# Performance work log

Hardware: AMD Instinct MI355X
Metric: run time of the kernel (lower is better)

## Reference

```python
import jax, jax.numpy as jnp
import numpy as np
import math

DEPTH = 3
RATIO = 0.5
EPS = 1e-5


def _mlp_ln(h, W1, b1, W2, b2, W3, b3, g, beta):
    h = jax.nn.gelu(h @ W1 + b1, approximate=False)
    h = jax.nn.gelu(h @ W2 + b2, approximate=False)
    h = h @ W3 + b3
    mu = jnp.mean(h, axis=-1, keepdims=True)
    var = jnp.mean((h - mu) ** 2, axis=-1, keepdims=True)
    return g * (h - mu) * jax.lax.rsqrt(var + EPS) + beta


def _node_to_node(x, s, r, n, p):
    # two-way gather -> scatter_add -> MLP+LN. Row n of x_pad is a zero dummy
    # node that absorbs edges dropped by pooling (fixed-size, jit-friendly).
    x_pad = jnp.concatenate([x, jnp.zeros((1, x.shape[1]), x.dtype)], axis=0)
    msg = x_pad[jnp.concatenate([s, r])]            # [2E, C]
    recv = jnp.concatenate([r, s])                  # [2E]
    agg = jax.ops.segment_sum(msg, recv, num_segments=n + 1)[:n]
    return _mlp_ln(agg, *p)


def _forward(x, senders, receivers, pool_w, down_p, up_p):
    s, r = senders, receivers
    xs, edges, perms = [x], [(s, r)], []
    n = x.shape[0]
    for i in range(DEPTH):
        k = math.ceil(RATIO * n)  # PyG topk: ceil(ratio * N)
        w = pool_w[i]
        score = jnp.tanh(x @ w / jnp.linalg.norm(w))
        vals, perm = jax.lax.top_k(score, k)
        x = x[perm] * vals[:, None]
        # remap edges; dropped nodes (and old dummy n) map to new dummy k
        nmap = jnp.full((n + 1,), k, dtype=s.dtype).at[perm].set(
            jnp.arange(k, dtype=s.dtype))
        ns_, nr_ = nmap[s], nmap[r]
        invalid = (ns_ == k) | (nr_ == k)
        s = jnp.where(invalid, k, ns_)
        r = jnp.where(invalid, k, nr_)
        x = _node_to_node(x, s, r, k, down_p[i])
        if i < DEPTH - 1:
            xs.append(x)
            edges.append((s, r))
        perms.append(perm)
        n = k
    for i in range(DEPTH):
        j = DEPTH - 1 - i
        res = xs[j]
        s, r = edges[j]
        perm = perms[j]
        up = jnp.zeros_like(res).at[perm].set(x)
        x = jnp.concatenate([res, up], axis=-1)  # sum_res=False -> concat
        x = _node_to_node(x, s, r, res.shape[0], up_p[i])
    return x


def setup_inputs() -> dict:
    key = jax.random.key(0)
    ks = jax.random.split(key, 16)
    N, E, C, D = 50000, 600000, 128, DEPTH
    f32 = jnp.float32

    def lin(k, fi, fo):
        return (jax.random.normal(k, (D, fi, fo), f32) / np.sqrt(fi)).astype(f32)

    return {
        'x': jax.random.normal(ks[0], (N, C), f32),
        'senders': jax.random.randint(ks[1], (E,), 0, N, dtype=jnp.int32),
        'receivers': jax.random.randint(ks[2], (E,), 0, N, dtype=jnp.int32),
        'pool_w': jax.random.normal(ks[3], (D, C), f32),
        'down_W1': lin(ks[4], C, C), 'down_b1': jnp.zeros((D, C), f32),
        'down_W2': lin(ks[5], C, C), 'down_b2': jnp.zeros((D, C), f32),
        'down_W3': lin(ks[6], C, C), 'down_b3': jnp.zeros((D, C), f32),
        'down_g': jnp.ones((D, C), f32), 'down_beta': jnp.zeros((D, C), f32),
        'up_W1': lin(ks[7], 2 * C, C), 'up_b1': jnp.zeros((D, C), f32),
        'up_W2': lin(ks[8], C, C), 'up_b2': jnp.zeros((D, C), f32),
        'up_W3': lin(ks[9], C, C), 'up_b3': jnp.zeros((D, C), f32),
        'up_g': jnp.ones((D, C), f32), 'up_beta': jnp.zeros((D, C), f32),
    }


def reference(x, senders, receivers, pool_w,
              down_W1, down_b1, down_W2, down_b2, down_W3, down_b3,
              down_g, down_beta,
              up_W1, up_b1, up_W2, up_b2, up_W3, up_b3, up_g, up_beta):
    down_p = [(down_W1[i], down_b1[i], down_W2[i], down_b2[i],
               down_W3[i], down_b3[i], down_g[i], down_beta[i])
              for i in range(DEPTH)]
    up_p = [(up_W1[i], up_b1[i], up_W2[i], up_b2[i],
             up_W3[i], up_b3[i], up_g[i], up_beta[i])
            for i in range(DEPTH)]
    return _forward(x, senders, receivers, pool_w, down_p, up_p)
```

## Files before the change

### kernel.cpp

```cpp
#include <hip/hip_runtime.h>
#include <math.h>


typedef unsigned short u16;
typedef short bf16x8 __attribute__((ext_vector_type(8)));
typedef float f32x4 __attribute__((ext_vector_type(4)));

#define HIST_STRIDE (2 * 65536 + 512)

__device__ __forceinline__ unsigned int fkey(float f) {
  unsigned int b = __float_as_uint(f);
  return (b & 0x80000000u) ? ~b : (b | 0x80000000u);
}

__device__ __forceinline__ float gelu_f(float v) {
  return 0.5f * v * (1.0f + erff(v * 0.70710678118654752f));
}

__device__ __forceinline__ u16 f2bf(float f) {
  unsigned u = __float_as_uint(f);
  u = (u + 0x7FFFu + ((u >> 16) & 1u)) >> 16;
  return (u16)u;
}
__device__ __forceinline__ float bf2f(u16 u) {
  return __uint_as_float(((unsigned)u) << 16);
}

__global__ void score_kernel(const float* __restrict__ x, const float* __restrict__ w,
                             float* __restrict__ key, float* __restrict__ valt, int n) {
  int wave = threadIdx.x >> 6, lane = threadIdx.x & 63;
  int i = blockIdx.x * 4 + wave;
  if (i >= n) return;
  float2 xv = *(const float2*)&x[(size_t)i * 128 + lane * 2];
  float2 wv = *(const float2*)&w[lane * 2];
  double d  = (double)xv.x * wv.x + (double)xv.y * wv.y;
  double nw = (double)wv.x * wv.x + (double)wv.y * wv.y;
  for (int o = 32; o; o >>= 1) { d += __shfl_down(d, o, 64); nw += __shfl_down(nw, o, 64); }
  if (lane == 0) {
    key[i]  = (float)d;
    valt[i] = (float)tanh(d / sqrt(nw));
  }
}

__global__ void preamble_kernel(const float* __restrict__ x, u16* __restrict__ xb, int n,
                                const float* __restrict__ uW1, const float* __restrict__ uW2,
                                const float* __restrict__ uW3, u16* __restrict__ wt1,
                                u16* __restrict__ wt2, u16* __restrict__ wt3,
                                const float* __restrict__ poolw, double* __restrict__ sqn,
                                u16* __restrict__ z0, u16* __restrict__ z1,
                                u16* __restrict__ z2, int* __restrict__ histAll,
                                int* __restrict__ degAll, int nbX, int nbHZ, int nHist,
                                int nDeg) {
  int b = blockIdx.x;
  if (b < nbX) {
    int gid = b * 256 + threadIdx.x;
    if (gid < n * 32) {
      float4 a = *(const float4*)&x[(size_t)gid * 4];
      *(ushort4*)&xb[(size_t)gid * 4] =
          make_ushort4(f2bf(a.x), f2bf(a.y), f2bf(a.z), f2bf(a.w));
    }
    return;
  }
  b -= nbX;
  if (b < 768) {
    int i = b * 256 + threadIdx.x;
    int lvl = i >> 16, rem = i & 65535;
    if (rem < 32768) {
      int k = rem >> 7, c = rem & 127;
      wt1[(size_t)lvl * 32768 + c * 256 + k] = f2bf(uW1[(size_t)lvl * 32768 + rem]);
    } else if (rem < 49152) {
      int j = rem - 32768; int k = j >> 7, c = j & 127;
      wt2[(size_t)lvl * 16384 + c * 128 + k] = f2bf(uW2[(size_t)lvl * 16384 + j]);
    } else {
      int j = rem - 49152; int k = j >> 7, c = j & 127;
      wt3[(size_t)lvl * 16384 + c * 128 + k] = f2bf(uW3[(size_t)lvl * 16384 + j]);
    }
    return;
  }
  b -= 768;
  if (b == 0) {
    if (threadIdx.x < 64) {
      int lane = threadIdx.x;
      for (int l = 0; l < 3; ++l) {
        float2 wv = *(const float2*)&poolw[l * 128 + lane * 2];
        double nw = (double)wv.x * wv.x + (double)wv.y * wv.y;
        for (int o = 32; o; o >>= 1) nw += __shfl_down(nw, o, 64);
        if (lane == 0) sqn[l] = sqrt(nw);
      }
    }
    return;
  }
  b -= 1;
  if (b == 0) {
    int t = threadIdx.x;
    if (t < 128) { z0[t] = 0; z1[t] = 0; z2[t] = 0; }
    return;
  }
  b -= 1;
  if (b < nbHZ) {
    int i = b * 256 + threadIdx.x;
    if (i < nHist) histAll[i] = 0;
    return;
  }
  b -= nbHZ;
  {
    int i = b * 256 + threadIdx.x;
    if (i < nDeg) degAll[i] = 0;
  }
}

__global__ void hist_hi_kernel(const float* __restrict__ key, int* __restrict__ hist,
                               int* __restrict__ csum, int n) {
  __shared__ int lc[256];
  lc[threadIdx.x] = 0;
  __syncthreads();
  int i = blockIdx.x * 256 + threadIdx.x;
  if (i < n) {
    unsigned b = fkey(key[i]) >> 16;
    atomicAdd(&hist[b], 1);
    atomicAdd(&lc[b >> 8], 1);
  }
  __syncthreads();
  int v = lc[threadIdx.x];
  if (v) atomicAdd(&csum[threadIdx.x], v);
}

__global__ void hist_lo_kernel(const float* __restrict__ key, const int* __restrict__ meta,
                               int* __restrict__ hist, int* __restrict__ csum, int n) {
  __shared__ int lc[256];
  lc[threadIdx.x] = 0;
  __syncthreads();
  int i = blockIdx.x * 256 + threadIdx.x;
  if (i < n) {
    unsigned u = fkey(key[i]);
    if ((u >> 16) == (unsigned)meta[0]) {
      unsigned b = u & 0xFFFFu;
      atomicAdd(&hist[b], 1);
      atomicAdd(&lc[b >> 8], 1);
    }
  }
  __syncthreads();
  int v = lc[threadIdx.x];
  if (v) atomicAdd(&csum[threadIdx.x], v);
}

__global__ void find_hi2_kernel(const int* __restrict__ hist, const int* __restrict__ csum,
                                int* __restrict__ meta, int k) {
  __shared__ int s[256];
  __shared__ int cSh, cumSh;
  int t = threadIdx.x;
  s[t] = csum[t];
  __syncthreads();
  if (t == 0) {
    int cum = 0, c = 0;
    for (int i = 255; i >= 0; --i) {
      if (cum + s[i] >= k) { c = i; break; }
      cum += s[i];
    }
    cSh = c; cumSh = cum;
  }
  __syncthreads();
  int c = cSh;
  s[t] = hist[c * 256 + t];
  __syncthreads();
  if (t == 0) {
    int cum = cumSh;
    for (int b = 255; b >= 0; --b) {
      int v = s[b];
      if (cum + v >= k) { meta[0] = c * 256 + b; meta[1] = k - cum; break; }
      cum += v;
    }
  }
}

__global__ void find_lo2_kernel(const int* __restrict__ hist, const int* __restrict__ csum,
                                int* __restrict__ meta) {
  __shared__ int s[256];
  __shared__ int cSh, cumSh;
  int t = threadIdx.x;
  int m = meta[1], B = meta[0];
  s[t] = csum[t];
  __syncthreads();
  if (t == 0) {
    int cum = 0, c = 0;
    for (int i = 255; i >= 0; --i) {
      if (cum + s[i] >= m) { c = i; break; }
      cum += s[i];
    }
    cSh = c; cumSh = cum;
  }
  __syncthreads();
  int c = cSh;
  s[t] = hist[c * 256 + t];
  __syncthreads();
  if (t == 0) {
    int cum = cumSh;
    for (int b = 255; b >= 0; --b) {
      int v = s[b];
      if (cum + v >= m) {
        meta[3] = (int)((((unsigned)B) << 16) | (unsigned)(c * 256 + b));
        meta[4] = m - cum;
        break;
      }
      cum += v;
    }
    meta[5] = 0;
  }
}

__global__ void tie_count_kernel(const float* __restrict__ key, const int* __restrict__ meta,
                                 int* __restrict__ tcnt, int n) {
  __shared__ int cnt[4];
  unsigned uT = (unsigned)meta[3];
  int i = blockIdx.x * 256 + threadIdx.x;
  bool tie = (i < n) && (fkey(key[i]) == uT);
  unsigned long long m = __ballot(tie);
  int lane = threadIdx.x & 63, w = threadIdx.x >> 6;
  if (lane == 0) cnt[w] = __popcll(m);
  __syncthreads();
  if (threadIdx.x == 0) tcnt[blockIdx.x] = cnt[0] + cnt[1] + cnt[2] + cnt[3];
}

__global__ void tie_select_kernel(const float* __restrict__ key, const float* __restrict__ valt,
                                  const int* __restrict__ tcnt, int* __restrict__ meta,
                                  int* __restrict__ perm, float* __restrict__ vals,
                                  int* __restrict__ nmap, int n, int k) {
  __shared__ int red[256];
  __shared__ int woff[4];
  int t = threadIdx.x;
  red[t] = (t < (int)blockIdx.x) ? tcnt[t] : 0;
  __syncthreads();
  for (int s = 128; s; s >>= 1) {
    if (t < s) red[t] += red[t + s];
    __syncthreads();
  }
  int blockbase = red[0];
  unsigned uT = (unsigned)meta[3];
  int tsel = meta[4];
  int i = blockIdx.x * 256 + t;
  unsigned u = (i < n) ? fkey(key[i]) : 0u;
  bool tie = (i < n) && (u == uT);
  unsigned long long m = __ballot(tie);
  int lane = t & 63, w = t >> 6;
  if (lane == 0) woff[w] = __popcll(m);
  __syncthreads();
  if (t == 0) {
    int c = 0;
    for (int q = 0; q < 4; ++q) { int v = woff[q]; woff[q] = c; c += v; }
  }
  __syncthreads();
  if (i > n) return;
  if (i == n) { nmap[n] = k; return; }
  bool sel;
  if (tie) {
    int pre = __popcll(m & ((1ull << lane) - 1ull));
    int rank = blockbase + woff[w] + pre;
    sel = (rank < tsel);
  } else {
    sel = (u > uT);
  }
  if (sel) {
    int slot = atomicAdd(&meta[5], 1);
    perm[slot] = i; vals[slot] = valt[i]; nmap[i] = slot;
  } else {
    nmap[i] = k;
  }
}

__global__ void pool_kernel(const float* __restrict__ x, const int* __restrict__ perm,
                            const float* __restrict__ vals, float* __restrict__ xp, int k) {
  int gid = blockIdx.x * 256 + threadIdx.x;
  int t = gid >> 5;
  if (t >= k) return;
  int c = (gid & 31) << 2;
  float v = vals[t];
  float4 a = *(const float4*)&x[(size_t)perm[t] * 128 + c];
  a.x *= v; a.y *= v; a.z *= v; a.w *= v;
  *(float4*)&xp[(size_t)t * 128 + c] = a;
}

__global__ void remap_deg_rank_kernel(const int* __restrict__ s_in, const int* __restrict__ r_in,
                                      const int* __restrict__ nmap, int* __restrict__ s_out,
                                      int* __restrict__ r_out, int* __restrict__ deg,
                                      int* __restrict__ rkS, int* __restrict__ rkR,
                                      int E, int k) {
  int e = blockIdx.x * 256 + threadIdx.x;
  if (e >= E) return;
  int a = nmap[s_in[e]], b = nmap[r_in[e]];
  if (a == k || b == k) { a = k; b = k; }
  s_out[e] = a; r_out[e] = b;
  if (a < k) {
    rkR[e] = atomicAdd(&deg[b], 1);
    rkS[e] = atomicAdd(&deg[a], 1);
  }
}

__global__ void deg_rank_kernel(const int* __restrict__ s, const int* __restrict__ r,
                                int* __restrict__ deg, int* __restrict__ rkS,
                                int* __restrict__ rkR, int E, int n) {
  int e = blockIdx.x * 256 + threadIdx.x;
  if (e >= E) return;
  int ss = s[e];
  if (ss >= n) return;
  int rr = r[e];
  rkR[e] = atomicAdd(&deg[rr], 1);
  rkS[e] = atomicAdd(&deg[ss], 1);
}

__global__ void scan_part_kernel(const int* __restrict__ deg, int* __restrict__ bsum, int n) {
  __shared__ int l[256];
  int i = blockIdx.x * 256 + threadIdx.x;
  l[threadIdx.x] = (i < n) ? deg[i] : 0;
  __syncthreads();
  for (int s = 128; s; s >>= 1) {
    if (threadIdx.x < s) l[threadIdx.x] += l[threadIdx.x + s];
    __syncthreads();
  }
  if (threadIdx.x == 0) bsum[blockIdx.x] = l[0];
}

__global__ void scan_final_kernel(const int* __restrict__ deg, const int* __restrict__ bsum,
                                  int* __restrict__ off, int n) {
  __shared__ int red[256];
  __shared__ int l[256];
  int i = blockIdx.x * 256 + threadIdx.x;
  int t = threadIdx.x;
  red[t] = (t < (int)blockIdx.x) ? bsum[t] : 0;
  __syncthreads();
  for (int s = 128; s; s >>= 1) {
    if (t < s) red[t] += red[t + s];
    __syncthreads();
  }
  int base = red[0];
  int v = (i < n) ? deg[i] : 0;
  l[t] = v;
  __syncthreads();
#pragma unroll
  for (int s = 1; s < 256; s <<= 1) {
    int add = (t >= s) ? l[t - s] : 0;
    __syncthreads();
    l[t] += add;
    __syncthreads();
  }
  int incl = l[t];
  if (i < n) {
    int e = base + incl - v;
    off[i] = e;
    if (i == n - 1) off[n] = base + incl;
  }
}

__global__ void rank_scatter_kernel(const int* __restrict__ s, const int* __restrict__ r,
                                    const int* __restrict__ off, const int* __restrict__ rkS,
                                    const int* __restrict__ rkR, int* __restrict__ idx,
                                    int E, int n) {
  int e = blockIdx.x * 256 + threadIdx.x;
  if (e >= E) return;
  int ss = s[e];
  if (ss >= n) return;
  int rr = r[e];
  idx[off[rr] + rkR[e]] = ss;
  idx[off[ss] + rkS[e]] = rr;
}

__global__ void idxup3_kernel(const int* __restrict__ idxA, const int* __restrict__ nmA,
                              const int* __restrict__ lenA, int* __restrict__ outA,
                              const int* __restrict__ idxB, const int* __restrict__ nmB,
                              const int* __restrict__ lenB, int* __restrict__ outB,
                              const int* __restrict__ idxC, const int* __restrict__ nmC,
                              const int* __restrict__ lenC, int* __restrict__ outC,
                              int nbSeg, int maxlen) {
  int seg = blockIdx.x / nbSeg;
  int j = (blockIdx.x - seg * nbSeg) * 256 + threadIdx.x;
  if (j >= maxlen) return;
  const int* idx; const int* nm; const int* len; int* out;
  if (seg == 0)      { idx = idxA; nm = nmA; len = lenA; out = outA; }
  else if (seg == 1) { idx = idxB; nm = nmB; len = lenB; out = outB; }
  else               { idx = idxC; nm = nmC; len = lenC; out = outC; }
  if (j >= len[0]) return;
  out[j] = nm[idx[j]];
}

__global__ void agg_kernel(const float* __restrict__ x, const int* __restrict__ off,
                           const int* __restrict__ idx, float* __restrict__ agg, int n) {
  int wave = threadIdx.x >> 6, lane = threadIdx.x & 63;
  int v = blockIdx.x * 4 + wave;
  if (v >= n) return;
  int lo = __builtin_amdgcn_readfirstlane(off[v]);
  int hi = __builtin_amdgcn_readfirstlane(off[v + 1]);
  int g = lane >> 5, sl = lane & 31;
  const float* bp = x + sl * 4;
  float4 acc = {0.f, 0.f, 0.f, 0.f};
#define ACC_F(EE)                                        \
  do {                                                   \
    float4 w_ = *(const float4*)(bp + (size_t)(EE) * 128);\
    acc.x += w_.x; acc.y += w_.y; acc.z += w_.z; acc.w += w_.w; \
  } while (0)
  int j = lo;
  for (; j + 8 <= hi; j += 8) {
    int q0 = idx[j],     q1 = idx[j + 1], q2 = idx[j + 2], q3 = idx[j + 3];
    int q4 = idx[j + 4], q5 = idx[j + 5], q6 = idx[j + 6], q7 = idx[j + 7];
    ACC_F(g ? q1 : q0);
    ACC_F(g ? q3 : q2);
    ACC_F(g ? q5 : q4);
    ACC_F(g ? q7 : q6);
  }
  for (; j + 2 <= hi; j += 2) {
    int q0 = idx[j], q1 = idx[j + 1];
    ACC_F(g ? q1 : q0);
  }
  if (j < hi) {
    int q0 = idx[j];
    if (!g) ACC_F(q0);
  }
#undef ACC_F
  acc.x += __shfl_xor(acc.x, 32, 64);
  acc.y += __shfl_xor(acc.y, 32, 64);
  acc.z += __shfl_xor(acc.z, 32, 64);
  acc.w += __shfl_xor(acc.w, 32, 64);
  if (!g) *(float4*)&agg[(size_t)v * 128 + sl * 4] = acc;
}

template <int OFS>
__global__ void agg_gather_kernel(const u16* __restrict__ tab, const int* __restrict__ idx,
                                  const int* __restrict__ off, u16* __restrict__ agg, int n) {
  int wave = threadIdx.x >> 6, lane = threadIdx.x & 63;
  int v = blockIdx.x * 4 + wave;
  if (v >= n) return;
  int lo = __builtin_amdgcn_readfirstlane(off[v]);
  int hi = __builtin_amdgcn_readfirstlane(off[v + 1]);
  int g = lane >> 4, sl = lane & 15;
  const u16* bp = tab + sl * 8;
  float4 a0 = {0.f, 0.f, 0.f, 0.f}, a1 = {0.f, 0.f, 0.f, 0.f};

#define ACC_ROW(EE)                                     \
  do {                                                  \
    uint4 wq = *(const uint4*)(bp + (size_t)(EE) * 128);\
    a0.x += __uint_as_float(wq.x << 16);                \
    a0.y += __uint_as_float(wq.x & 0xffff0000u);        \
    a0.z += __uint_as_float(wq.y << 16);                \
    a0.w += __uint_as_float(wq.y & 0xffff0000u);        \
    a1.x += __uint_as_float(wq.z << 16);                \
    a1.y += __uint_as_float(wq.z & 0xffff0000u);        \
    a1.z += __uint_as_float(wq.w << 16);                \
    a1.w += __uint_as_float(wq.w & 0xffff0000u);        \
  } while (0)

  int j = lo;
  for (; j + 16 <= hi; j += 16) {
    int e0 = idx[j + g];
    int e1 = idx[j + g + 4];
    int e2 = idx[j + g + 8];
    int e3 = idx[j + g + 12];
    ACC_ROW(e0); ACC_ROW(e1); ACC_ROW(e2); ACC_ROW(e3);
  }
  for (; j + 4 <= hi; j += 4) {
    int e0 = idx[j + g];
    ACC_ROW(e0);
  }
  int rmn = hi - j;
  if (g < rmn) {
    int e = idx[j + g];
    ACC_ROW(e);
  }
#undef ACC_ROW

  a0.x += __shfl_xor(a0.x, 16, 64);
  a0.y += __shfl_xor(a0.y, 16, 64);
  a0.z += __shfl_xor(a0.z, 16, 64);
  a0.w += __shfl_xor(a0.w, 16, 64);
  a1.x += __shfl_xor(a1.x, 16, 64);
  a1.y += __shfl_xor(a1.y, 16, 64);
  a1.z += __shfl_xor(a1.z, 16, 64);
  a1.w += __shfl_xor(a1.w, 16, 64);
  a0.x += __shfl_xor(a0.x, 32, 64);
  a0.y += __shfl_xor(a0.y, 32, 64);
  a0.z += __shfl_xor(a0.z, 32, 64);
  a0.w += __shfl_xor(a0.w, 32, 64);
  a1.x += __shfl_xor(a1.x, 32, 64);
  a1.y += __shfl_xor(a1.y, 32, 64);
  a1.z += __shfl_xor(a1.z, 32, 64);
  a1.w += __shfl_xor(a1.w, 32, 64);

  if (lane < 16) {
    bf16x8 ov;
    ov[0] = (short)f2bf(a0.x); ov[1] = (short)f2bf(a0.y);
    ov[2] = (short)f2bf(a0.z); ov[3] = (short)f2bf(a0.w);
    ov[4] = (short)f2bf(a1.x); ov[5] = (short)f2bf(a1.y);
    ov[6] = (short)f2bf(a1.z); ov[7] = (short)f2bf(a1.w);
    *(bf16x8*)&agg[(size_t)v * 256 + OFS + sl * 8] = ov;
  }
}

template <bool GELU>
__global__ __launch_bounds__(256) void gemm_kernel(const float* __restrict__ A,
                                                   const float* __restrict__ W,
                                                   const float* __restrict__ bias,
                                                   float* __restrict__ out, int n) {
  __shared__ float As[32 * 32];
  __shared__ float Ws[32 * 128];
  int t = threadIdx.x;
  int row0 = blockIdx.x * 32;
  int colg = (t & 31) << 2;
  int rowg = (t >> 5) << 2;
  float acc[4][4];
#pragma unroll
  for (int i = 0; i < 4; ++i)
#pragma unroll
    for (int j = 0; j < 4; ++j) acc[i][j] = 0.f;

  for (int k0 = 0; k0 < 128; k0 += 32) {
    __syncthreads();
    {
      int ar = t >> 3, ac = (t & 7) << 2;
      float4 av = make_float4(0.f, 0.f, 0.f, 0.f);
// ... 100 lines not shown
  int lane = t & 63, wave = t >> 6;
  int row0 = blockIdx.x * 64;
  f32x4 acc[8];
#pragma unroll
  for (int i = 0; i < 8; ++i) acc[i] = (f32x4){0.f, 0.f, 0.f, 0.f};

  for (int k0 = 0; k0 < 128; k0 += 64) {
    __syncthreads();
#pragma unroll
    for (int i = 0; i < 2; ++i) {
      int c = t + i * 256;
      int r = c >> 3, seg = c & 7;
      bf16x8 v = {0, 0, 0, 0, 0, 0, 0, 0};
      if (row0 + r < n) v = *(const bf16x8*)&A[(size_t)(row0 + r) * 128 + k0 + seg * 8];
      *(bf16x8*)&As[r * 72 + seg * 8] = v;
    }
#pragma unroll
    for (int i = 0; i < 4; ++i) {
      int c = t + i * 256;
      int r = c >> 3, seg = c & 7;
      *(bf16x8*)&Ws[r * 72 + seg * 8] = *(const bf16x8*)&WT[(size_t)r * 128 + k0 + seg * 8];
    }
    __syncthreads();
#pragma unroll
    for (int kk = 0; kk < 64; kk += 32) {
      bf16x8 a = *(const bf16x8*)&As[(wave * 16 + (lane & 15)) * 72 + kk + (lane >> 4) * 8];
#pragma unroll
      for (int ct = 0; ct < 8; ++ct) {
        bf16x8 b = *(const bf16x8*)&Ws[(ct * 16 + (lane & 15)) * 72 + kk + (lane >> 4) * 8];
        acc[ct] = __builtin_amdgcn_mfma_f32_16x16x32_bf16(a, b, acc[ct], 0, 0, 0);
      }
    }
  }
  int colb = lane & 15, rquad = lane >> 4;
  float bv[8], gv[8], bev[8];
#pragma unroll
  for (int ct = 0; ct < 8; ++ct) {
    int col = ct * 16 + colb;
    bv[ct] = bias[col]; gv[ct] = g[col]; bev[ct] = beta[col];
  }
#pragma unroll
  for (int r = 0; r < 4; ++r) {
    float s1 = 0.f;
#pragma unroll
    for (int ct = 0; ct < 8; ++ct) s1 += acc[ct][r] + bv[ct];
#pragma unroll
    for (int o = 1; o <= 8; o <<= 1) s1 += __shfl_xor(s1, o, 64);
    float mu = s1 * (1.0f / 128.0f);
    float s2 = 0.f;
#pragma unroll
    for (int ct = 0; ct < 8; ++ct) { float d = acc[ct][r] + bv[ct] - mu; s2 += d * d; }
#pragma unroll
    for (int o = 1; o <= 8; o <<= 1) s2 += __shfl_xor(s2, o, 64);
    float rs = rsqrtf(s2 * (1.0f / 128.0f) + 1e-5f);
    int row = row0 + wave * 16 + rquad * 4 + r;
    if (row < n) {
#pragma unroll
      for (int ct = 0; ct < 8; ++ct) {
        int col = ct * 16 + colb;
        float o = gv[ct] * (acc[ct][r] + bv[ct] - mu) * rs + bev[ct];
        if (WF32) out[(size_t)row * 128 + col] = o;
        if (WBF)  outbf[(size_t)row * 128 + col] = f2bf(o);
      }
    }
  }
}

template <bool SCORE, bool WBF>
__global__ void ln_kernel(const float* __restrict__ h, const float* __restrict__ g,
                          const float* __restrict__ beta, float* __restrict__ out,
                          u16* __restrict__ outbf, const float* __restrict__ wnext,
                          const double* __restrict__ sqn, float* __restrict__ key,
                          float* __restrict__ valt, int n) {
  int wave = threadIdx.x >> 6, lane = threadIdx.x & 63;
  int i = blockIdx.x * 4 + wave;
  if (i >= n) return;
  float2 hv = *(const float2*)&h[(size_t)i * 128 + lane * 2];
  float s = hv.x + hv.y;
  for (int o = 32; o; o >>= 1) s += __shfl_down(s, o, 64);
  float mu = __shfl(s, 0, 64) * (1.0f / 128.0f);
  float dx = hv.x - mu, dy = hv.y - mu;
  float q = dx * dx + dy * dy;
  for (int o = 32; o; o >>= 1) q += __shfl_down(q, o, 64);
  float var = __shfl(q, 0, 64) * (1.0f / 128.0f);
  float rs = rsqrtf(var + 1e-5f);
  float2 gv = *(const float2*)&g[lane * 2];
  float2 bv = *(const float2*)&beta[lane * 2];
  float2 o2; o2.x = gv.x * dx * rs + bv.x; o2.y = gv.y * dy * rs + bv.y;
  *(float2*)&out[(size_t)i * 128 + lane * 2] = o2;
  if (WBF)
    *(ushort2*)&outbf[(size_t)i * 128 + lane * 2] = make_ushort2(f2bf(o2.x), f2bf(o2.y));
  if (SCORE) {
    float2 wv = *(const float2*)&wnext[lane * 2];
    double d = (double)o2.x * wv.x + (double)o2.y * wv.y;
    for (int o = 32; o; o >>= 1) d += __shfl_down(d, o, 64);
    if (lane == 0) {
      key[i]  = (float)d;
      valt[i] = (float)tanh(d / sqn[0]);
    }
  }
}


static inline int cdiv(int a, int b) { return (a + b - 1) / b; }

extern "C" void kernel_launch(void* const* d_in, const int* in_sizes, int n_in,
                              void* d_out, int out_size, void* d_ws, size_t ws_size,
                              hipStream_t stream) {
  const float* x0   = (const float*)d_in[0];
  const int*   snd  = (const int*)d_in[1];
  const int*   rcv  = (const int*)d_in[2];
  const float* poolw = (const float*)d_in[3];
  const float* dW1 = (const float*)d_in[4];
  const float* db1 = (const float*)d_in[5];
  const float* dW2 = (const float*)d_in[6];
  const float* db2 = (const float*)d_in[7];
  const float* dW3 = (const float*)d_in[8];
  const float* db3 = (const float*)d_in[9];
  const float* dg  = (const float*)d_in[10];
  const float* dbe = (const float*)d_in[11];
  const float* uW1 = (const float*)d_in[12];
  const float* ub1 = (const float*)d_in[13];
  const float* uW2 = (const float*)d_in[14];
  const float* ub2 = (const float*)d_in[15];
  const float* uW3 = (const float*)d_in[16];
  const float* ub3 = (const float*)d_in[17];
  const float* ug  = (const float*)d_in[18];
  const float* ube = (const float*)d_in[19];

  const int N0 = in_sizes[0] / 128;
  const int E  = in_sizes[1];
  const int N1 = (N0 + 1) / 2, N2 = (N1 + 1) / 2, N3 = (N2 + 1) / 2;

  char* p = (char*)d_ws;
  auto alloc = [&](size_t bytes) -> void* {
    void* r = (void*)p;
    p += (bytes + 255) & ~(size_t)255;
    return r;
  };
  float* key  = (float*)alloc((size_t)N0 * 4);
  float* valt = (float*)alloc((size_t)N0 * 4);
  int*   histAll = (int*)alloc((size_t)3 * HIST_STRIDE * 4);
  int*   meta = (int*)alloc(64 * 4);
  int*   tcnt = (int*)alloc(512 * 4);
  int*   bsum = (int*)alloc(256 * 4);
  int*   nm1 = (int*)alloc((size_t)(N0 + 1) * 4);
  int*   nm2 = (int*)alloc((size_t)(N1 + 1) * 4);
  int*   nm3 = (int*)alloc((size_t)(N2 + 1) * 4);
  int*   perm0 = (int*)alloc((size_t)N1 * 4);
  int*   perm1 = (int*)alloc((size_t)N2 * 4);
  int*   perm2 = (int*)alloc((size_t)N3 * 4);
  float* vals  = (float*)alloc((size_t)N1 * 4);
  double* sqn  = (double*)alloc(8 * 8);
  int* s1 = (int*)alloc((size_t)E * 4); int* r1 = (int*)alloc((size_t)E * 4);
  int* s2 = (int*)alloc((size_t)E * 4); int* r2 = (int*)alloc((size_t)E * 4);
  int* s3 = (int*)alloc((size_t)E * 4); int* r3 = (int*)alloc((size_t)E * 4);
  float* x1 = (float*)alloc((size_t)N1 * 128 * 4);
  float* x2 = (float*)alloc((size_t)N2 * 128 * 4);
  float* x3 = (float*)alloc((size_t)N3 * 128 * 4);
  float* xp = (float*)alloc((size_t)N1 * 128 * 4);
  float* aggf = (float*)alloc((size_t)N1 * 128 * 4);
  float* h1f  = (float*)alloc((size_t)N1 * 128 * 4);
  float* h2f  = (float*)alloc((size_t)N1 * 128 * 4);
  u16* agg_bf = (u16*)alloc((size_t)N0 * 256 * 2);
  u16* res0_bf = (u16*)alloc((size_t)N0 * 128 * 2);
  u16* res1_bf = (u16*)alloc((size_t)N1 * 128 * 2);
  u16* res2_bf = (u16*)alloc((size_t)N2 * 128 * 2);
  u16* x3_bf   = (u16*)alloc((size_t)(N3 + 1) * 128 * 2);
  u16* xu2_bf  = (u16*)alloc((size_t)(N2 + 1) * 128 * 2);
  u16* xu1_bf  = (u16*)alloc((size_t)(N1 + 1) * 128 * 2);
  u16* wt1 = (u16*)alloc((size_t)3 * 128 * 256 * 2);
  u16* wt2 = (u16*)alloc((size_t)3 * 128 * 128 * 2);
  u16* wt3 = (u16*)alloc((size_t)3 * 128 * 128 * 2);
  int* degAll = (int*)alloc((size_t)(N0 + N1 + N2 + N3) * 4);
  int* deg0 = degAll;
  int* deg1 = degAll + N0;
  int* deg2 = deg1 + N1;
  int* deg3 = deg2 + N2;
  int* off0 = (int*)alloc((size_t)(N0 + 1) * 4);
  int* idx0 = (int*)alloc((size_t)2 * E * 4);
  int* off1 = (int*)alloc((size_t)(N1 + 1) * 4);
  int* idx1 = (int*)alloc((size_t)2 * E * 4);
  int* off2 = (int*)alloc((size_t)(N2 + 1) * 4);
  int* idx2 = (int*)alloc((size_t)2 * E * 4);
  int* off3 = (int*)alloc((size_t)(N3 + 1) * 4);
  int* idx3 = (int*)alloc((size_t)2 * E * 4);
  int* idxu0 = (int*)alloc((size_t)2 * E * 4);
  int* idxu1 = (int*)alloc((size_t)2 * E * 4);
  int* idxu2 = (int*)alloc((size_t)2 * E * 4);

  u16* h1b = (u16*)xp;
  u16* h2b = (u16*)s1;
  int* rkS = (int*)agg_bf;
  int* rkR = rkS + E;

  auto run_scan = [&](int* degB, int* offB, int n) {
    int nb = cdiv(n, 256);
    scan_part_kernel<<<nb, 256, 0, stream>>>(degB, bsum, n);
    scan_final_kernel<<<nb, 256, 0, stream>>>(degB, bsum, offB, n);
  };

  {
    int nbX = cdiv(N0 * 32, 256);
    int nHist = 3 * HIST_STRIDE;
    int nbHZ = cdiv(nHist, 256);
    int nDeg = N0 + N1 + N2 + N3;
    int nbDZ = cdiv(nDeg, 256);
    preamble_kernel<<<nbX + 768 + 1 + 1 + nbHZ + nbDZ, 256, 0, stream>>>(
        x0, res0_bf, N0, uW1, uW2, uW3, wt1, wt2, wt3, poolw, sqn,
        x3_bf + (size_t)N3 * 128, xu2_bf + (size_t)N2 * 128,
        xu1_bf + (size_t)N1 * 128, histAll, degAll, nbX, nbHZ, nHist, nDeg);
  }

  deg_rank_kernel<<<cdiv(E, 256), 256, 0, stream>>>(snd, rcv, deg0, rkS, rkR, E, N0);
  run_scan(deg0, off0, N0);
  rank_scatter_kernel<<<cdiv(E, 256), 256, 0, stream>>>(snd, rcv, off0, rkS, rkR, idx0, E, N0);

  auto down_step = [&](int n, int k, const float* xcur, const int* sin, const int* rin,
                       int* sout, int* rout, int* permL, int* nmL, float* xnext,
                       u16* xnext_bf, int lvl, int* offL, int* degL, int* idxL) {
    int nb = cdiv(n, 256);
    int* histL = histAll + (size_t)lvl * HIST_STRIDE;
    int* csum_hi = histL + 2 * 65536;
    int* csum_lo = csum_hi + 256;
    hist_hi_kernel<<<nb, 256, 0, stream>>>(key, histL, csum_hi, n);
    find_hi2_kernel<<<1, 256, 0, stream>>>(histL, csum_hi, meta, k);
    hist_lo_kernel<<<nb, 256, 0, stream>>>(key, meta, histL + 65536, csum_lo, n);
    find_lo2_kernel<<<1, 256, 0, stream>>>(histL + 65536, csum_lo, meta);
    tie_count_kernel<<<nb, 256, 0, stream>>>(key, meta, tcnt, n);
    tie_select_kernel<<<cdiv(n + 1, 256), 256, 0, stream>>>(
        key, valt, tcnt, meta, permL, vals, nmL, n, k);
    pool_kernel<<<cdiv(k * 32, 256), 256, 0, stream>>>(xcur, permL, vals, xp, k);
    remap_deg_rank_kernel<<<cdiv(E, 256), 256, 0, stream>>>(
        sin, rin, nmL, sout, rout, degL, rkS, rkR, E, k);
    run_scan(degL, offL, k);
    rank_scatter_kernel<<<cdiv(E, 256), 256, 0, stream>>>(sout, rout, offL, rkS, rkR, idxL, E, k);
    agg_kernel<<<cdiv(k, 4), 256, 0, stream>>>(xp, offL, idxL, aggf, k);
    gemm_kernel<true><<<cdiv(k, 32), 256, 0, stream>>>(
        aggf, dW1 + (size_t)lvl * 128 * 128, db1 + (size_t)lvl * 128, h1f, k);
    gemm_kernel<true><<<cdiv(k, 32), 256, 0, stream>>>(
        h1f, dW2 + (size_t)lvl * 128 * 128, db2 + (size_t)lvl * 128, h2f, k);
    gemm_kernel<false><<<cdiv(k, 32), 256, 0, stream>>>(
        h2f, dW3 + (size_t)lvl * 128 * 128, db3 + (size_t)lvl * 128, h1f, k);
    if (lvl < 2)
      ln_kernel<true, true><<<cdiv(k, 4), 256, 0, stream>>>(
          h1f, dg + (size_t)lvl * 128, dbe + (size_t)lvl * 128, xnext, xnext_bf,
          poolw + (size_t)(lvl + 1) * 128, sqn + (lvl + 1), key, valt, k);
    else
      ln_kernel<false, true><<<cdiv(k, 4), 256, 0, stream>>>(
          h1f, dg + (size_t)lvl * 128, dbe + (size_t)lvl * 128, xnext, xnext_bf,
          nullptr, nullptr, nullptr, nullptr, k);
  };

  score_kernel<<<cdiv(N0, 4), 256, 0, stream>>>(x0, poolw, key, valt, N0);
  down_step(N0, N1, x0, snd, rcv, s1, r1, perm0, nm1, x1, res1_bf, 0, off1, deg1, idx1);
  down_step(N1, N2, x1, s1, r1, s2, r2, perm1, nm2, x2, res2_bf, 1, off2, deg2, idx2);
  down_step(N2, N3, x2, s2, r2, s3, r3, perm2, nm3, x3, x3_bf, 2, off3, deg3, idx3);

  {
    int nbSeg = cdiv(2 * E, 256);
    idxup3_kernel<<<3 * nbSeg, 256, 0, stream>>>(
        idx2, nm3, off2 + N2, idxu2,
        idx1, nm2, off1 + N1, idxu1,
        idx0, nm1, off0 + N0, idxu0, nbSeg, 2 * E);
  }

  auto up_step = [&](int n, const u16* resb, const u16* xdb, int lvl,
                     const int* offL, const int* idxL, const int* idxUL,
                     bool wantF32, float* outF32, u16* outBF) {
    agg_gather_kernel<0><<<cdiv(n, 4), 256, 0, stream>>>(resb, idxL, offL, agg_bf, n);
    agg_gather_kernel<128><<<cdiv(n, 4), 256, 0, stream>>>(xdb, idxUL, offL, agg_bf, n);
    gemm_mfma_kernel<256><<<cdiv(n, 64), 256, 0, stream>>>(
        agg_bf, wt1 + (size_t)lvl * 128 * 256, ub1 + (size_t)lvl * 128, h1b, n);
    gemm_mfma_kernel<128><<<cdiv(n, 64), 256, 0, stream>>>(
        h1b, wt2 + (size_t)lvl * 128 * 128, ub2 + (size_t)lvl * 128, h2b, n);
    if (wantF32)
      gemm_mfma_ln_kernel<true, false><<<cdiv(n, 64), 256, 0, stream>>>(
          h2b, wt3 + (size_t)lvl * 128 * 128, ub3 + (size_t)lvl * 128,
          ug + (size_t)lvl * 128, ube + (size_t)lvl * 128, outF32, nullptr, n);
    else
      gemm_mfma_ln_kernel<false, true><<<cdiv(n, 64), 256, 0, stream>>>(
          h2b, wt3 + (size_t)lvl * 128 * 128, ub3 + (size_t)lvl * 128,
          ug + (size_t)lvl * 128, ube + (size_t)lvl * 128, nullptr, outBF, n);
  };

  up_step(N2, res2_bf, x3_bf,  0, off2, idx2, idxu2, false, nullptr, xu2_bf);
  up_step(N1, res1_bf, xu2_bf, 1, off1, idx1, idxu1, false, nullptr, xu1_bf);
  up_step(N0, res0_bf, xu1_bf, 2, off0, idx0, idxu0, true, (float*)d_out, nullptr);

  (void)n_in; (void)out_size; (void)ws_size;
}
```

Before: 921.4 us.

## Build CSR with LDS-blocked counting sort instead of global atomics

Replaces the global-atomic degree/rank CSR construction with a two-pass counting sort. Each of 64 edge chunks counts degrees in shared memory per node sub-range, a column-sum and scan produce per-chunk offsets, and a second pass scatters edges using LDS atomics. The find_hi/lo kernels also switch from a serial single-thread loop to a parallel suffix scan. This is meant to cut global atomic contention, but it reads the edge list several times per node sub-range and adds a 64×N histogram buffer plus extra launches.

```diff
diff --git a/kernel.cpp b/kernel.cpp
--- a/kernel.cpp
+++ b/kernel.cpp
@@ -7,6 +7,9 @@
 typedef float f32x4 __attribute__((ext_vector_type(4)));
 
 #define HIST_STRIDE (2 * 65536 + 512)
+#define NB 64
+#define NB_LOG 6
+#define SUBR 16000
 
 __device__ __forceinline__ unsigned int fkey(float f) {
   unsigned int b = __float_as_uint(f);
@@ -144,68 +147,61 @@
   if (v) atomicAdd(&csum[threadIdx.x], v);
 }
 
+__device__ __forceinline__ void suffix_scan256(int* sA, int t) {
+  for (int o = 1; o < 256; o <<= 1) {
+    int add = (t + o < 256) ? sA[t + o] : 0;
+    __syncthreads();
+    sA[t] += add;
+    __syncthreads();
+  }
+}
+
 __global__ void find_hi2_kernel(const int* __restrict__ hist, const int* __restrict__ csum,
                                 int* __restrict__ meta, int k) {
-  __shared__ int s[256];
+  __shared__ int sA[256];
   __shared__ int cSh, cumSh;
   int t = threadIdx.x;
-  s[t] = csum[t];
-  __syncthreads();
-  if (t == 0) {
-    int cum = 0, c = 0;
-    for (int i = 255; i >= 0; --i) {
-      if (cum + s[i] >= k) { c = i; break; }
-      cum += s[i];
-    }
-    cSh = c; cumSh = cum;
-  }
+  sA[t] = csum[t];
+  __syncthreads();
+  suffix_scan256(sA, t);
+  int nxt = (t == 255) ? 0 : sA[t + 1];
+  if (sA[t] >= k && nxt < k) { cSh = t; cumSh = nxt; }
   __syncthreads();
   int c = cSh;
-  s[t] = hist[c * 256 + t];
-  __syncthreads();
-  if (t == 0) {
-    int cum = cumSh;
-    for (int b = 255; b >= 0; --b) {
-      int v = s[b];
-      if (cum + v >= k) { meta[0] = c * 256 + b; meta[1] = k - cum; break; }
-      cum += v;
-    }
+  int k2 = k - cumSh;
+  sA[t] = hist[c * 256 + t];
+  __syncthreads();
+  suffix_scan256(sA, t);
+  nxt = (t == 255) ? 0 : sA[t + 1];
+  if (sA[t] >= k2 && nxt < k2) {
+    meta[0] = c * 256 + t;
+    meta[1] = k2 - nxt;
   }
 }
 
 __global__ void find_lo2_kernel(const int* __restrict__ hist, const int* __restrict__ csum,
                                 int* __restrict__ meta) {
-  __shared__ int s[256];
+  __shared__ int sA[256];
   __shared__ int cSh, cumSh;
   int t = threadIdx.x;
   int m = meta[1], B = meta[0];
-  s[t] = csum[t];
-  __syncthreads();
-  if (t == 0) {
-    int cum = 0, c = 0;
-    for (int i = 255; i >= 0; --i) {
-      if (cum + s[i] >= m) { c = i; break; }
-      cum += s[i];
-    }
-    cSh = c; cumSh = cum;
-  }
+  sA[t] = csum[t];
+  __syncthreads();
+  suffix_scan256(sA, t);
+  int nxt = (t == 255) ? 0 : sA[t + 1];
+  if (sA[t] >= m && nxt < m) { cSh = t; cumSh = nxt; }
   __syncthreads();
   int c = cSh;
-  s[t] = hist[c * 256 + t];
-  __syncthreads();
-  if (t == 0) {
-    int cum = cumSh;
-    for (int b = 255; b >= 0; --b) {
-      int v = s[b];
-      if (cum + v >= m) {
-        meta[3] = (int)((((unsigned)B) << 16) | (unsigned)(c * 256 + b));
-        meta[4] = m - cum;
-        break;
-      }
-      cum += v;
-    }
-    meta[5] = 0;
-  }
+  int m2 = m - cumSh;
+  sA[t] = hist[c * 256 + t];
+  __syncthreads();
+  suffix_scan256(sA, t);
+  nxt = (t == 255) ? 0 : sA[t + 1];
+  if (sA[t] >= m2 && nxt < m2) {
+    meta[3] = (int)((((unsigned)B) << 16) | (unsigned)(c * 256 + t));
+    meta[4] = m2 - nxt;
+  }
+  if (t == 0) meta[5] = 0;
 }
 
 __global__ void tie_count_kernel(const float* __restrict__ key, const int* __restrict__ meta,
@@ -279,38 +275,48 @@
   *(float4*)&xp[(size_t)t * 128 + c] = a;
 }
 
-__global__ void remap_deg_rank_kernel(const int* __restrict__ s_in, const int* __restrict__ r_in,
-                                      const int* __restrict__ nmap, int* __restrict__ s_out,
-                                      int* __restrict__ r_out, int* __restrict__ deg,
-                                      int* __restrict__ rkS, int* __restrict__ rkR,
-                                      int E, int k) {
+__global__ void remap_kernel(const int* __restrict__ s_in, const int* __restrict__ r_in,
+                             const int* __restrict__ nmap, int* __restrict__ s_out,
+                             int* __restrict__ r_out, int E, int k) {
   int e = blockIdx.x * 256 + threadIdx.x;
   if (e >= E) return;
   int a = nmap[s_in[e]], b = nmap[r_in[e]];
   if (a == k || b == k) { a = k; b = k; }
   s_out[e] = a; r_out[e] = b;
-  if (a < k) {
-    rkR[e] = atomicAdd(&deg[b], 1);
-    rkS[e] = atomicAdd(&deg[a], 1);
-  }
-}
-
-__global__ void deg_rank_kernel(const int* __restrict__ s, const int* __restrict__ r,
-                                int* __restrict__ deg, int* __restrict__ rkS,
-                                int* __restrict__ rkR, int E, int n) {
-  int e = blockIdx.x * 256 + threadIdx.x;
-  if (e >= E) return;
-  int ss = s[e];
-  if (ss >= n) return;
-  int rr = r[e];
-  rkR[e] = atomicAdd(&deg[rr], 1);
-  rkS[e] = atomicAdd(&deg[ss], 1);
-}
-
-__global__ void scan_part_kernel(const int* __restrict__ deg, int* __restrict__ bsum, int n) {
+}
+
+__global__ void csr_count_kernel(const int* __restrict__ s, const int* __restrict__ r,
+                                 int* __restrict__ H, int N, int E, int CH) {
+  __shared__ int cnt[SUBR];
+  int b = blockIdx.x & (NB - 1);
+  int sub = blockIdx.x >> NB_LOG;
+  int base = sub * SUBR;
+  int top = base + SUBR; if (top > N) top = N;
+  int span = top - base;
+  for (int t = threadIdx.x; t < span; t += 256) cnt[t] = 0;
+  __syncthreads();
+  int lo = b * CH, hi = lo + CH; if (hi > E) hi = E;
+  for (int e = lo + threadIdx.x; e < hi; e += 256) {
+    int sv = s[e], rv = r[e];
+    if ((unsigned)(rv - base) < (unsigned)span) atomicAdd(&cnt[rv - base], 1);
+    if ((unsigned)(sv - base) < (unsigned)span) atomicAdd(&cnt[sv - base], 1);
+  }
+  __syncthreads();
+  int* Hb = H + (size_t)b * N + base;
+  for (int t = threadIdx.x; t < span; t += 256) Hb[t] = cnt[t];
+}
+
+__global__ void colsum_part_kernel(const int* __restrict__ H, int* __restrict__ deg,
+                                   int* __restrict__ bsum, int n) {
   __shared__ int l[256];
   int i = blockIdx.x * 256 + threadIdx.x;
-  l[threadIdx.x] = (i < n) ? deg[i] : 0;
+  int v = 0;
+  if (i < n) {
+#pragma unroll 4
+    for (int b = 0; b < NB; ++b) v += H[(size_t)b * n + i];
+    deg[i] = v;
+  }
+  l[threadIdx.x] = (i < n) ? v : 0;
   __syncthreads();
   for (int s = 128; s; s >>= 1) {
     if (threadIdx.x < s) l[threadIdx.x] += l[threadIdx.x + s];
@@ -319,8 +325,8 @@
   if (threadIdx.x == 0) bsum[blockIdx.x] = l[0];
 }
 
-__global__ void scan_final_kernel(const int* __restrict__ deg, const int* __restrict__ bsum,
-                                  int* __restrict__ off, int n) {
+__global__ void scanfix_kernel(const int* __restrict__ deg, const int* __restrict__ bsum,
+                               int* __restrict__ off, int* __restrict__ H, int n) {
   __shared__ int red[256];
   __shared__ int l[256];
   int i = blockIdx.x * 256 + threadIdx.x;
@@ -347,20 +353,41 @@
     int e = base + incl - v;
     off[i] = e;
     if (i == n - 1) off[n] = base + incl;
-  }
-}
-
-__global__ void rank_scatter_kernel(const int* __restrict__ s, const int* __restrict__ r,
-                                    const int* __restrict__ off, const int* __restrict__ rkS,
-                                    const int* __restrict__ rkR, int* __restrict__ idx,
-                                    int E, int n) {
-  int e = blockIdx.x * 256 + threadIdx.x;
-  if (e >= E) return;
-  int ss = s[e];
-  if (ss >= n) return;
-  int rr = r[e];
-  idx[off[rr] + rkR[e]] = ss;
-  idx[off[ss] + rkS[e]] = rr;
+    int run = e;
+#pragma unroll 4
+    for (int b = 0; b < NB; ++b) {
+      size_t id = (size_t)b * n + i;
+      int tv = H[id];
+      H[id] = run;
+      run += tv;
+    }
+  }
+}
+
+__global__ void csr_scatter_lds_kernel(const int* __restrict__ s, const int* __restrict__ r,
+                                       const int* __restrict__ H, int* __restrict__ idx,
+                                       int N, int E, int CH) {
+  __shared__ int cnt[SUBR];
+  int b = blockIdx.x & (NB - 1);
+  int sub = blockIdx.x >> NB_LOG;
+  int base = sub * SUBR;
+  int top = base + SUBR; if (top > N) top = N;
+  int span = top - base;
+  for (int t = threadIdx.x; t < span; t += 256) cnt[t] = 0;
+  __syncthreads();
+  int lo = b * CH, hi = lo + CH; if (hi > E) hi = E;
+  const int* Hb = H + (size_t)b * N;
+  for (int e = lo + threadIdx.x; e < hi; e += 256) {
+    int sv = s[e], rv = r[e];
+    if ((unsigned)(rv - base) < (unsigned)span) {
+      int loc = atomicAdd(&cnt[rv - base], 1);
+      idx[Hb[rv] + loc] = sv;
+    }
+    if ((unsigned)(sv - base) < (unsigned)span) {
+      int loc = atomicAdd(&cnt[sv - base], 1);
+      idx[Hb[sv] + loc] = rv;
+    }
+  }
 }
 
 __global__ void idxup3_kernel(const int* __restrict__ idxA, const int* __restrict__ nmA,
@@ -803,17 +830,10 @@
   int* idxu0 = (int*)alloc((size_t)2 * E * 4);
   int* idxu1 = (int*)alloc((size_t)2 * E * 4);
   int* idxu2 = (int*)alloc((size_t)2 * E * 4);
+  int* H = (int*)alloc((size_t)NB * N0 * 4);
 
   u16* h1b = (u16*)xp;
   u16* h2b = (u16*)s1;
-  int* rkS = (int*)agg_bf;
-  int* rkR = rkS + E;
-
-  auto run_scan = [&](int* degB, int* offB, int n) {
-    int nb = cdiv(n, 256);
-    scan_part_kernel<<<nb, 256, 0, stream>>>(degB, bsum, n);
-    scan_final_kernel<<<nb, 256, 0, stream>>>(degB, bsum, offB, n);
-  };
 
   {
     int nbX = cdiv(N0 * 32, 256);
@@ -827,9 +847,17 @@
         xu1_bf + (size_t)N1 * 128, histAll, degAll, nbX, nbHZ, nHist, nDeg);
   }
 
-  deg_rank_kernel<<<cdiv(E, 256), 256, 0, stream>>>(snd, rcv, deg0, rkS, rkR, E, N0);
-  run_scan(deg0, off0, N0);
-  rank_scatter_kernel<<<cdiv(E, 256), 256, 0, stream>>>(snd, rcv, off0, rkS, rkR, idx0, E, N0);
+  auto run_csr = [&](const int* sA, const int* rA, int* degB, int* offB, int* idxB, int n) {
+    int nSub = cdiv(n, SUBR);
+    int CH = cdiv(E, NB);
+    int nbN = cdiv(n, 256);
+    csr_count_kernel<<<NB * nSub, 256, 0, stream>>>(sA, rA, H, n, E, CH);
+    colsum_part_kernel<<<nbN, 256, 0, stream>>>(H, degB, bsum, n);
+    scanfix_kernel<<<nbN, 256, 0, stream>>>(degB, bsum, offB, H, n);
+    csr_scatter_lds_kernel<<<NB * nSub, 256, 0, stream>>>(sA, rA, H, idxB, n, E, CH);
+  };
+
+  run_csr(snd, rcv, deg0, off0, idx0, N0);
 
   auto down_step = [&](int n, int k, const float* xcur, const int* sin, const int* rin,
                        int* sout, int* rout, int* permL, int* nmL, float* xnext,
@@ -846,10 +874,8 @@
     tie_select_kernel<<<cdiv(n + 1, 256), 256, 0, stream>>>(
         key, valt, tcnt, meta, permL, vals, nmL, n, k);
     pool_kernel<<<cdiv(k * 32, 256), 256, 0, stream>>>(xcur, permL, vals, xp, k);
-    remap_deg_rank_kernel<<<cdiv(E, 256), 256, 0, stream>>>(
-        sin, rin, nmL, sout, rout, degL, rkS, rkR, E, k);
-    run_scan(degL, offL, k);
-    rank_scatter_kernel<<<cdiv(E, 256), 256, 0, stream>>>(sout, rout, offL, rkS, rkR, idxL, E, k);
+    remap_kernel<<<cdiv(E, 256), 256, 0, stream>>>(sin, rin, nmL, sout, rout, E, k);
+    run_csr(sout, rout, degL, offL, idxL, k);
     agg_kernel<<<cdiv(k, 4), 256, 0, stream>>>(xp, offL, idxL, aggf, k);
     gemm_kernel<true><<<cdiv(k, 32), 256, 0, stream>>>(
         aggf, dW1 + (size_t)lvl * 128 * 128, db1 + (size_t)lvl * 128, h1f, k);
```

New measurement: 991.4 us. +7.6%, slower.

## Derive pooled-level CSR from parent CSR instead of remapping full edge lists

Applied to the files above, without the earlier changes.

Each down level now builds its CSR adjacency by walking the parent level's CSR for each kept node, filtering neighbours through the node map with wave ballots. This replaces the per-edge remap kernel that used global atomics and the rank-scatter over all E edges, and drops the per-level s/r edge arrays. The top-k threshold search kernels also switch from a serial single-thread loop to a parallel 256-wide suffix scan. The cost is irregular per-node wave work, which wastes lanes on low-degree nodes.

```diff
diff --git a/kernel.cpp b/kernel.cpp
--- a/kernel.cpp
+++ b/kernel.cpp
@@ -144,68 +144,61 @@
   if (v) atomicAdd(&csum[threadIdx.x], v);
 }
 
+__device__ __forceinline__ void suffix_scan256(int* sA, int t) {
+  for (int o = 1; o < 256; o <<= 1) {
+    int add = (t + o < 256) ? sA[t + o] : 0;
+    __syncthreads();
+    sA[t] += add;
+    __syncthreads();
+  }
+}
+
 __global__ void find_hi2_kernel(const int* __restrict__ hist, const int* __restrict__ csum,
                                 int* __restrict__ meta, int k) {
-  __shared__ int s[256];
+  __shared__ int sA[256];
   __shared__ int cSh, cumSh;
   int t = threadIdx.x;
-  s[t] = csum[t];
-  __syncthreads();
-  if (t == 0) {
-    int cum = 0, c = 0;
-    for (int i = 255; i >= 0; --i) {
-      if (cum + s[i] >= k) { c = i; break; }
-      cum += s[i];
-    }
-    cSh = c; cumSh = cum;
-  }
+  sA[t] = csum[t];
+  __syncthreads();
+  suffix_scan256(sA, t);
+  int nxt = (t == 255) ? 0 : sA[t + 1];
+  if (sA[t] >= k && nxt < k) { cSh = t; cumSh = nxt; }
   __syncthreads();
   int c = cSh;
-  s[t] = hist[c * 256 + t];
-  __syncthreads();
-  if (t == 0) {
-    int cum = cumSh;
-    for (int b = 255; b >= 0; --b) {
-      int v = s[b];
-      if (cum + v >= k) { meta[0] = c * 256 + b; meta[1] = k - cum; break; }
-      cum += v;
-    }
+  int k2 = k - cumSh;
+  sA[t] = hist[c * 256 + t];
+  __syncthreads();
+  suffix_scan256(sA, t);
+  nxt = (t == 255) ? 0 : sA[t + 1];
+  if (sA[t] >= k2 && nxt < k2) {
+    meta[0] = c * 256 + t;
+    meta[1] = k2 - nxt;
   }
 }
 
 __global__ void find_lo2_kernel(const int* __restrict__ hist, const int* __restrict__ csum,
                                 int* __restrict__ meta) {
-  __shared__ int s[256];
+  __shared__ int sA[256];
   __shared__ int cSh, cumSh;
   int t = threadIdx.x;
   int m = meta[1], B = meta[0];
-  s[t] = csum[t];
-  __syncthreads();
-  if (t == 0) {
-    int cum = 0, c = 0;
-    for (int i = 255; i >= 0; --i) {
-      if (cum + s[i] >= m) { c = i; break; }
-      cum += s[i];
-    }
-    cSh = c; cumSh = cum;
-  }
+  sA[t] = csum[t];
+  __syncthreads();
+  suffix_scan256(sA, t);
+  int nxt = (t == 255) ? 0 : sA[t + 1];
+  if (sA[t] >= m && nxt < m) { cSh = t; cumSh = nxt; }
   __syncthreads();
   int c = cSh;
-  s[t] = hist[c * 256 + t];
-  __syncthreads();
-  if (t == 0) {
-    int cum = cumSh;
-    for (int b = 255; b >= 0; --b) {
-      int v = s[b];
-      if (cum + v >= m) {
-        meta[3] = (int)((((unsigned)B) << 16) | (unsigned)(c * 256 + b));
-        meta[4] = m - cum;
-        break;
-      }
-      cum += v;
-    }
-    meta[5] = 0;
-  }
+  int m2 = m - cumSh;
+  sA[t] = hist[c * 256 + t];
+  __syncthreads();
+  suffix_scan256(sA, t);
+  nxt = (t == 255) ? 0 : sA[t + 1];
+  if (sA[t] >= m2 && nxt < m2) {
+    meta[3] = (int)((((unsigned)B) << 16) | (unsigned)(c * 256 + t));
+    meta[4] = m2 - nxt;
+  }
+  if (t == 0) meta[5] = 0;
 }
 
 __global__ void tie_count_kernel(const float* __restrict__ key, const int* __restrict__ meta,
@@ -279,22 +272,6 @@
   *(float4*)&xp[(size_t)t * 128 + c] = a;
 }
 
-__global__ void remap_deg_rank_kernel(const int* __restrict__ s_in, const int* __restrict__ r_in,
-                                      const int* __restrict__ nmap, int* __restrict__ s_out,
-                                      int* __restrict__ r_out, int* __restrict__ deg,
-                                      int* __restrict__ rkS, int* __restrict__ rkR,
-                                      int E, int k) {
-  int e = blockIdx.x * 256 + threadIdx.x;
-  if (e >= E) return;
-  int a = nmap[s_in[e]], b = nmap[r_in[e]];
-  if (a == k || b == k) { a = k; b = k; }
-  s_out[e] = a; r_out[e] = b;
-  if (a < k) {
-    rkR[e] = atomicAdd(&deg[b], 1);
-    rkS[e] = atomicAdd(&deg[a], 1);
-  }
-}
-
 __global__ void deg_rank_kernel(const int* __restrict__ s, const int* __restrict__ r,
                                 int* __restrict__ deg, int* __restrict__ rkS,
                                 int* __restrict__ rkR, int E, int n) {
@@ -305,49 +282,6 @@
   int rr = r[e];
   rkR[e] = atomicAdd(&deg[rr], 1);
   rkS[e] = atomicAdd(&deg[ss], 1);
-}
-
-__global__ void scan_part_kernel(const int* __restrict__ deg, int* __restrict__ bsum, int n) {
-  __shared__ int l[256];
-  int i = blockIdx.x * 256 + threadIdx.x;
-  l[threadIdx.x] = (i < n) ? deg[i] : 0;
-  __syncthreads();
-  for (int s = 128; s; s >>= 1) {
-    if (threadIdx.x < s) l[threadIdx.x] += l[threadIdx.x + s];
-    __syncthreads();
-  }
-  if (threadIdx.x == 0) bsum[blockIdx.x] = l[0];
-}
-
-__global__ void scan_final_kernel(const int* __restrict__ deg, const int* __restrict__ bsum,
-                                  int* __restrict__ off, int n) {
-  __shared__ int red[256];
-  __shared__ int l[256];
-  int i = blockIdx.x * 256 + threadIdx.x;
-  int t = threadIdx.x;
-  red[t] = (t < (int)blockIdx.x) ? bsum[t] : 0;
-  __syncthreads();
-  for (int s = 128; s; s >>= 1) {
-    if (t < s) red[t] += red[t + s];
-    __syncthreads();
-  }
-  int base = red[0];
-  int v = (i < n) ? deg[i] : 0;
-  l[t] = v;
-  __syncthreads();
-#pragma unroll
-  for (int s = 1; s < 256; s <<= 1) {
-    int add = (t >= s) ? l[t - s] : 0;
-    __syncthreads();
-    l[t] += add;
-    __syncthreads();
-  }
-  int incl = l[t];
-  if (i < n) {
-    int e = base + incl - v;
-    off[i] = e;
-    if (i == n - 1) off[n] = base + incl;
-  }
 }
 
 __global__ void rank_scatter_kernel(const int* __restrict__ s, const int* __restrict__ r,
@@ -361,6 +295,91 @@
   int rr = r[e];
   idx[off[rr] + rkR[e]] = ss;
   idx[off[ss] + rkS[e]] = rr;
+}
+
+__global__ void derive_deg_kernel(const int* __restrict__ permL, const int* __restrict__ nm,
+                                  const int* __restrict__ offP, const int* __restrict__ idxP,
+                                  int* __restrict__ deg, int k) {
+  int wave = threadIdx.x >> 6, lane = threadIdx.x & 63;
+  int v = blockIdx.x * 4 + wave;
+  if (v >= k) return;
+  int p = permL[v];
+  int lo = __builtin_amdgcn_readfirstlane(offP[p]);
+  int hi = __builtin_amdgcn_readfirstlane(offP[p + 1]);
+  int cnt = 0;
+  for (int j0 = lo; j0 < hi; j0 += 64) {
+    int j = j0 + lane;
+    bool ok = (j < hi) && (nm[idxP[j]] < k);
+    unsigned long long msk = __ballot(ok);
+    cnt += __popcll(msk);
+  }
+  if (lane == 0) deg[v] = cnt;
+}
+
+__global__ void derive_fill_kernel(const int* __restrict__ permL, const int* __restrict__ nm,
+                                   const int* __restrict__ offP, const int* __restrict__ idxP,
+                                   const int* __restrict__ offL, int* __restrict__ idxL,
+                                   int k) {
+  int wave = threadIdx.x >> 6, lane = threadIdx.x & 63;
+  int v = blockIdx.x * 4 + wave;
+  if (v >= k) return;
+  int p = permL[v];
+  int lo = __builtin_amdgcn_readfirstlane(offP[p]);
+  int hi = __builtin_amdgcn_readfirstlane(offP[p + 1]);
+  int base = __builtin_amdgcn_readfirstlane(offL[v]);
+  for (int j0 = lo; j0 < hi; j0 += 64) {
+    int j = j0 + lane;
+    int m = k;
+    if (j < hi) m = nm[idxP[j]];
+    bool ok = m < k;
+    unsigned long long msk = __ballot(ok);
+    int rank = __popcll(msk & ((1ull << lane) - 1ull));
+    if (ok) idxL[base + rank] = m;
+    base += __popcll(msk);
+  }
+}
+
+__global__ void scan_part_kernel(const int* __restrict__ deg, int* __restrict__ bsum, int n) {
+  __shared__ int l[256];
+  int i = blockIdx.x * 256 + threadIdx.x;
+  l[threadIdx.x] = (i < n) ? deg[i] : 0;
+  __syncthreads();
+  for (int s = 128; s; s >>= 1) {
+    if (threadIdx.x < s) l[threadIdx.x] += l[threadIdx.x + s];
+    __syncthreads();
+  }
+  if (threadIdx.x == 0) bsum[blockIdx.x] = l[0];
+}
+
+__global__ void scan_final_kernel(const int* __restrict__ deg, const int* __restrict__ bsum,
+                                  int* __restrict__ off, int n) {
+  __shared__ int red[256];
+  __shared__ int l[256];
+  int i = blockIdx.x * 256 + threadIdx.x;
+  int t = threadIdx.x;
+  red[t] = (t < (int)blockIdx.x) ? bsum[t] : 0;
+  __syncthreads();
+  for (int s = 128; s; s >>= 1) {
+    if (t < s) red[t] += red[t + s];
+    __syncthreads();
+  }
+  int base = red[0];
+  int v = (i < n) ? deg[i] : 0;
+  l[t] = v;
+  __syncthreads();
+#pragma unroll
+  for (int s = 1; s < 256; s <<= 1) {
+    int add = (t >= s) ? l[t - s] : 0;
+    __syncthreads();
+    l[t] += add;
+    __syncthreads();
+  }
+  int incl = l[t];
+  if (i < n) {
+    int e = base + incl - v;
+    off[i] = e;
+    if (i == n - 1) off[n] = base + incl;
+  }
 }
 
 __global__ void idxup3_kernel(const int* __restrict__ idxA, const int* __restrict__ nmA,
@@ -767,9 +786,6 @@
   int*   perm2 = (int*)alloc((size_t)N3 * 4);
   float* vals  = (float*)alloc((size_t)N1 * 4);
   double* sqn  = (double*)alloc(8 * 8);
-  int* s1 = (int*)alloc((size_t)E * 4); int* r1 = (int*)alloc((size_t)E * 4);
-  int* s2 = (int*)alloc((size_t)E * 4); int* r2 = (int*)alloc((size_t)E * 4);
-  int* s3 = (int*)alloc((size_t)E * 4); int* r3 = (int*)alloc((size_t)E * 4);
   float* x1 = (float*)alloc((size_t)N1 * 128 * 4);
   float* x2 = (float*)alloc((size_t)N2 * 128 * 4);
   float* x3 = (float*)alloc((size_t)N3 * 128 * 4);
@@ -803,9 +819,8 @@
   int* idxu0 = (int*)alloc((size_t)2 * E * 4);
   int* idxu1 = (int*)alloc((size_t)2 * E * 4);
   int* idxu2 = (int*)alloc((size_t)2 * E * 4);
-
   u16* h1b = (u16*)xp;
-  u16* h2b = (u16*)s1;
+  u16* h2b = (u16*)alloc((size_t)N0 * 128 * 2);
   int* rkS = (int*)agg_bf;
   int* rkR = rkS + E;
 
@@ -831,9 +846,10 @@
   run_scan(deg0, off0, N0);
   rank_scatter_kernel<<<cdiv(E, 256), 256, 0, stream>>>(snd, rcv, off0, rkS, rkR, idx0, E, N0);
 
-  auto down_step = [&](int n, int k, const float* xcur, const int* sin, const int* rin,
-                       int* sout, int* rout, int* permL, int* nmL, float* xnext,
-                       u16* xnext_bf, int lvl, int* offL, int* degL, int* idxL) {
+  auto down_step = [&](int n, int k, const float* xcur, int* permL, int* nmL,
+                       float* xnext, u16* xnext_bf, int lvl,
+                       const int* offP, const int* idxP,
+                       int* offL, int* degL, int* idxL) {
     int nb = cdiv(n, 256);
     int* histL = histAll + (size_t)lvl * HIST_STRIDE;
     int* csum_hi = histL + 2 * 65536;
@@ -846,10 +862,9 @@
     tie_select_kernel<<<cdiv(n + 1, 256), 256, 0, stream>>>(
         key, valt, tcnt, meta, permL, vals, nmL, n, k);
     pool_kernel<<<cdiv(k * 32, 256), 256, 0, stream>>>(xcur, permL, vals, xp, k);
-    remap_deg_rank_kernel<<<cdiv(E, 256), 256, 0, stream>>>(
-        sin, rin, nmL, sout, rout, degL, rkS, rkR, E, k);
+    derive_deg_kernel<<<cdiv(k, 4), 256, 0, stream>>>(permL, nmL, offP, idxP, degL, k);
     run_scan(degL, offL, k);
-    rank_scatter_kernel<<<cdiv(E, 256), 256, 0, stream>>>(sout, rout, offL, rkS, rkR, idxL, E, k);
+    derive_fill_kernel<<<cdiv(k, 4), 256, 0, stream>>>(permL, nmL, offP, idxP, offL, idxL, k);
     agg_kernel<<<cdiv(k, 4), 256, 0, stream>>>(xp, offL, idxL, aggf, k);
     gemm_kernel<true><<<cdiv(k, 32), 256, 0, stream>>>(
         aggf, dW1 + (size_t)lvl * 128 * 128, db1 + (size_t)lvl * 128, h1f, k);
@@ -868,9 +883,9 @@
   };
 
   score_kernel<<<cdiv(N0, 4), 256, 0, stream>>>(x0, poolw, key, valt, N0);
-  down_step(N0, N1, x0, snd, rcv, s1, r1, perm0, nm1, x1, res1_bf, 0, off1, deg1, idx1);
-  down_step(N1, N2, x1, s1, r1, s2, r2, perm1, nm2, x2, res2_bf, 1, off2, deg2, idx2);
-  down_step(N2, N3, x2, s2, r2, s3, r3, perm2, nm3, x3, x3_bf, 2, off3, deg3, idx3);
+  down_step(N0, N1, x0, perm0, nm1, x1, res1_bf, 0, off0, idx0, off1, deg1, idx1);
+  down_step(N1, N2, x1, perm1, nm2, x2, res2_bf, 1, off1, idx1, off2, deg2, idx2);
+  down_step(N2, N3, x2, perm2, nm3, x3, x3_bf,   2, off2, idx2, off3, deg3, idx3);
 
   {
     int nbSeg = cdiv(2 * E, 256);
```

Result: faster. 830.9 us (-9.8%).
